# Optimization experiments

Hardware: AMD Instinct MI355X
Metric: run time of the kernel (lower is better)

Reference implementation:

```python
import jax, jax.numpy as jnp
import numpy as np

BATCH = 65536
SEQ_LEN = 32
EMB = 64
H = 128


def setup_inputs() -> dict:
    key = jax.random.key(0)
    ks = jax.random.split(key, 12)
    s = 0.05
    inp = {
        "last_pos": jax.random.normal(ks[0], (BATCH, 2), jnp.float32),
        "last_pos_rel": jax.random.normal(ks[1], (BATCH, 2), jnp.float32),
        "hh": jax.random.normal(ks[2], (1, BATCH, H), jnp.float32),
        "ch": jax.random.normal(ks[3], (1, BATCH, H), jnp.float32),
        "seq_start_end": jnp.sort(jax.random.randint(ks[4], (256, 2), 0, BATCH), axis=0),
        # LSTM(embedding_dim -> h_dim), PyTorch gate order [i, f, g, o]
        "w_ih": jax.random.normal(ks[5], (4 * H, EMB), jnp.float32) * s,
        "w_hh": jax.random.normal(ks[6], (4 * H, H), jnp.float32) * s,
        "b_ih": jax.random.normal(ks[7], (4 * H,), jnp.float32) * s,
        "b_hh": jax.random.normal(ks[8], (4 * H,), jnp.float32) * s,
        # spatial_embedding: Linear(2 -> EMB)
        "w_emb": jax.random.normal(ks[9], (EMB, 2), jnp.float32) * s,
        "b_emb": jax.random.normal(ks[10], (EMB,), jnp.float32) * s,
        # hidden2pos: Linear(H -> 2)
        "w_pos": jax.random.normal(ks[11], (2, H), jnp.float32) * s,
        "b_pos": jnp.zeros((2,), jnp.float32),
    }
    return inp


def _decode(last_pos, last_pos_rel, hh, ch, w_ih, w_hh, b_ih, b_hh,
            w_emb, b_emb, w_pos, b_pos):
    h0, c0 = hh[0], ch[0]                      # (B, H)
    x0 = last_pos_rel @ w_emb.T + b_emb        # (B, EMB)
    b = b_ih + b_hh

    def step(carry, _):
        h, c, lp, x = carry
        gates = x @ w_ih.T + h @ w_hh.T + b    # (B, 4H)
        i, f, g, o = jnp.split(gates, 4, axis=-1)
        c2 = jax.nn.sigmoid(f) * c + jax.nn.sigmoid(i) * jnp.tanh(g)
        h2 = jax.nn.sigmoid(o) * jnp.tanh(c2)
        rel = h2 @ w_pos.T + b_pos             # (B, 2)
        cur = rel + lp
        x2 = rel @ w_emb.T + b_emb             # next decoder input embedding
        return (h2, c2, cur, x2), rel

    (hN, cN, _, _), rels = jax.lax.scan(step, (h0, c0, last_pos, x0),
                                        None, length=SEQ_LEN)
    # rels: (SEQ_LEN, B, 2) == pred_traj_fake_rel; hN[None]: (1, B, H)
    return rels, hN[None]


def reference(last_pos, last_pos_rel, hh, ch, seq_start_end,
              w_ih, w_hh, b_ih, b_hh, w_emb, b_emb, w_pos, b_pos):
    # seq_start_end is unused when pool_every_timestep=False
    return _decode(last_pos, last_pos_rel, hh, ch,
                   w_ih, w_hh, b_ih, b_hh, w_emb, b_emb, w_pos, b_pos)
```

## Files before the change

### kernel.cpp

```cpp
#include <hip/hip_runtime.h>

#define B_TOT 65536
#define SEQ   32

typedef __bf16 bf16_8 __attribute__((ext_vector_type(8)));
typedef __bf16 bf16_4 __attribute__((ext_vector_type(4)));
typedef float  float4v __attribute__((ext_vector_type(4)));
typedef float  float2v __attribute__((ext_vector_type(2)));

#define SC1 (-1.4426950408889634f)
#define SC2 (-2.8853900817779268f)

__device__ inline unsigned short f2bf(float f){
    unsigned u = __builtin_bit_cast(unsigned, f);
    u += 0x7FFFu + ((u >> 16) & 1u);
    return (unsigned short)(u >> 16);
}

__device__ inline float2v v_exp2(float2v x){
    float2v r; r[0] = __builtin_amdgcn_exp2f(x[0]); r[1] = __builtin_amdgcn_exp2f(x[1]); return r;
}
__device__ inline float2v v_rcp(float2v x){
    float2v r; r[0] = __builtin_amdgcn_rcpf(x[0]); r[1] = __builtin_amdgcn_rcpf(x[1]); return r;
}
__device__ inline float2v v_fma(float2v a, float2v b, float2v c){
    float2v r; r[0] = __builtin_fmaf(a[0], b[0], c[0]); r[1] = __builtin_fmaf(a[1], b[1], c[1]); return r;
}

__global__ void prep_kernel(const float* __restrict__ w_ih,
                            const float* __restrict__ w_hh,
                            const float* __restrict__ b_ih,
                            const float* __restrict__ b_hh,
                            const float* __restrict__ w_emb,
                            const float* __restrict__ b_emb,
                            const float* __restrict__ w_pos,
                            const float* __restrict__ b_pos,
                            unsigned short* __restrict__ weff,
                            float* __restrict__ beff,
                            float* __restrict__ m2,
                            unsigned short* __restrict__ wposA)
{
    int n = threadIdx.x;
    float m20 = 0.f, m21 = 0.f, bi = 0.f;
    for (int e = 0; e < 64; ++e){
        float wv = w_ih[n*64 + e];
        m20 += w_emb[e*2 + 0] * wv;
        m21 += w_emb[e*2 + 1] * wv;
        bi  += b_emb[e] * wv;
    }
    float sc = ((n >> 7) == 2) ? SC2 : SC1;
    m2[n]       = m20 * sc;
    m2[512 + n] = m21 * sc;
    beff[n] = (b_ih[n] + b_hh[n] + bi + b_pos[0]*m20 + b_pos[1]*m21) * sc;
    for (int k = 0; k < 128; ++k){
        float wv = w_hh[n*128 + k] + w_pos[k]*m20 + w_pos[128 + k]*m21;
        weff[n*128 + k] = f2bf(wv * sc);
    }
    if (n < 256) wposA[n] = f2bf(w_pos[n]);
    for (int idx = n; idx < 14*128; idx += 512) wposA[256 + idx] = 0;
}

__global__ __launch_bounds__(256, 1) void dec_kernel(
    const float* __restrict__ lpr,
    const float* __restrict__ hh,
    const float* __restrict__ ch,
    const float* __restrict__ b_pos,
    const unsigned short* __restrict__ wposA,
    const unsigned short* __restrict__ weff,
    const float* __restrict__ beff,
    const float* __restrict__ m2,
    float* __restrict__ out)
{
    __shared__ __align__(16) unsigned short lhA[16][152];
    __shared__ __align__(16) unsigned short lhB[16][152];
    __shared__ float ubuf[32][2];
    __shared__ __align__(16) float hsh[32][132];

    const int tid  = threadIdx.x;
    const int w    = tid >> 6;
    const int lane = tid & 63;
    const int q    = lane >> 4;
    const int l    = lane & 15;
    const int row0 = blockIdx.x << 5;
    const int batchA = row0 + l;
    const int batchB = row0 + 16 + l;

    const float2v one2 = {1.f, 1.f};
    const float2v sc22 = {SC2, SC2};

    bf16_8 wA[8][4];
    float4v bias4[8];
#pragma unroll
    for (int t8 = 0; t8 < 8; ++t8){
        int nbase = ((t8 >> 1) << 7) + 32*w + ((t8 & 1) << 4);
        int gA = nbase + l;
#pragma unroll
        for (int kt = 0; kt < 4; ++kt)
            wA[t8][kt] = *(const bf16_8*)(weff + (gA << 7) + kt*32 + (q << 3));
        bias4[t8] = *(const float4v*)(beff + nbase + (q << 2));
    }

    bf16_8 wpA[4];
#pragma unroll
    for (int kt = 0; kt < 4; ++kt)
        wpA[kt] = *(const bf16_8*)(wposA + (l << 7) + kt*32 + (q << 3));
    const float bp0 = b_pos[0], bp1 = b_pos[1];

    float2v cstA[2][2], cstB[2][2];
#pragma unroll
    for (int X = 0; X < 2; ++X){
        float4v ca = *(const float4v*)(ch + (batchA << 7) + 32*w + 16*X + (q << 2));
        float4v cb = *(const float4v*)(ch + (batchB << 7) + 32*w + 16*X + (q << 2));
        float2v t;
        t[0]=ca[0]; t[1]=ca[1]; cstA[X][0]=t;
        t[0]=ca[2]; t[1]=ca[3]; cstA[X][1]=t;
        t[0]=cb[0]; t[1]=cb[1]; cstB[X][0]=t;
        t[0]=cb[2]; t[1]=cb[3]; cstB[X][1]=t;
    }

    bf16_8 bA[4], bB[4];
#pragma unroll
    for (int kt = 0; kt < 4; ++kt){
        const float* pa = hh + (batchA << 7) + kt*32 + (q << 3);
        const float* pb = hh + (batchB << 7) + kt*32 + (q << 3);
        float4v a0 = *(const float4v*)pa;      float4v a1 = *(const float4v*)(pa + 4);
        float4v c0 = *(const float4v*)pb;      float4v c1 = *(const float4v*)(pb + 4);
        bf16_8 ta, tb;
        ta[0]=(__bf16)a0[0]; ta[1]=(__bf16)a0[1]; ta[2]=(__bf16)a0[2]; ta[3]=(__bf16)a0[3];
        ta[4]=(__bf16)a1[0]; ta[5]=(__bf16)a1[1]; ta[6]=(__bf16)a1[2]; ta[7]=(__bf16)a1[3];
        tb[0]=(__bf16)c0[0]; tb[1]=(__bf16)c0[1]; tb[2]=(__bf16)c0[2]; tb[3]=(__bf16)c0[3];
        tb[4]=(__bf16)c1[0]; tb[5]=(__bf16)c1[1]; tb[6]=(__bf16)c1[2]; tb[7]=(__bf16)c1[3];
        bA[kt] = ta;
        bB[kt] = tb;
    }

    if (w == 0){
        float4v r = {0.f, 0.f, 0.f, 0.f};
#pragma unroll
        for (int kt = 0; kt < 4; ++kt)
            r = __builtin_amdgcn_mfma_f32_16x16x32_bf16(wpA[kt], bA[kt], r, 0, 0, 0);
        if (q == 0){
            float2v lp = *(const float2v*)(lpr + (batchA << 1));
            ubuf[l][0] = lp[0] - (r[0] + bp0);
            ubuf[l][1] = lp[1] - (r[1] + bp1);
        }
    }
    if (w == 1){
        float4v r = {0.f, 0.f, 0.f, 0.f};
#pragma unroll
        for (int kt = 0; kt < 4; ++kt)
            r = __builtin_amdgcn_mfma_f32_16x16x32_bf16(wpA[kt], bB[kt], r, 0, 0, 0);
        if (q == 0){
            float2v lp = *(const float2v*)(lpr + (batchB << 1));
            ubuf[16 + l][0] = lp[0] - (r[0] + bp0);
            ubuf[16 + l][1] = lp[1] - (r[1] + bp1);
        }
    }
    __syncthreads();

    float4v accA[8], accB[8];

    auto do_gates = [&](float4v (&acc)[8], bf16_8 (&b)[4]){
#pragma unroll
        for (int t8 = 0; t8 < 8; ++t8)
            acc[t8] = __builtin_amdgcn_mfma_f32_16x16x32_bf16(wA[t8][0], b[0], bias4[t8], 0, 0, 0);
#pragma unroll
        for (int kt = 1; kt < 4; ++kt)
#pragma unroll
            for (int t8 = 0; t8 < 8; ++t8)
                acc[t8] = __builtin_amdgcn_mfma_f32_16x16x32_bf16(wA[t8][kt], b[kt], acc[t8], 0, 0, 0);
    };

    auto u0fix = [&](float4v (&acc)[8], int ur){
        float u0 = ubuf[ur][0], u1 = ubuf[ur][1];
#pragma unroll
        for (int t8 = 0; t8 < 8; ++t8){
            int g0 = ((t8 >> 1) << 7) + 32*w + ((t8 & 1) << 4) + (q << 2);
            float4v ma = *(const float4v*)(m2 + g0);
            float4v mb = *(const float4v*)(m2 + 512 + g0);
#pragma unroll
            for (int r4 = 0; r4 < 4; ++r4)
                acc[t8][r4] += u0*ma[r4] + u1*mb[r4];
        }
    };

    auto elem_write = [&](float4v (&acc)[8], float2v (&cst)[2][2],
                          unsigned short (*lhp)[152], bool finalh, int hrow){
#pragma unroll
        for (int X = 0; X < 2; ++X){
            bf16_4 hv;
#pragma unroll
            for (int p = 0; p < 2; ++p){
                float2v iv = {acc[0 + X][2*p], acc[0 + X][2*p + 1]};
                float2v fv = {acc[2 + X][2*p], acc[2 + X][2*p + 1]};
                float2v gv = {acc[4 + X][2*p], acc[4 + X][2*p + 1]};
                float2v ov = {acc[6 + X][2*p], acc[6 + X][2*p + 1]};
                float2v ei = v_exp2(iv);
                float2v ef = v_exp2(fv);
                float2v eg = v_exp2(gv);
                float2v pi_ = ei + one2;
                float2v pf  = ef + one2;
                float2v pg  = eg + one2;
                float2v mg  = one2 - eg;
                float2v t2  = pi_ * pg;
                float2v den = pf * t2;
                float2v num = v_fma(cst[X][p], t2, pf * mg);
                float2v c2  = num * v_rcp(den);
                float2v eo  = v_exp2(ov);
                float2v ec  = v_exp2(c2 * sc22);
                float2v po  = eo + one2;
                float2v pc  = ec + one2;
                float2v mc  = one2 - ec;
                float2v h2  = mc * v_rcp(po * pc);
                cst[X][p] = c2;
                hv[2*p]     = (__bf16)h2[0];
                hv[2*p + 1] = (__bf16)h2[1];
                if (finalh){
                    int cb = 32*w + 16*X + (q << 2) + 2*p;
                    hsh[hrow][cb]     = h2[0];
                    hsh[hrow][cb + 1] = h2[1];
                }
            }
            *(bf16_4*)&lhp[l][32*w + 16*X + (q << 2)] = hv;
        }
    };

    auto reload = [&](bf16_8 (&b)[4], const unsigned short (*lhp)[152]){
#pragma unroll
        for (int kt = 0; kt < 4; ++kt)
            b[kt] = *(const bf16_8*)&lhp[l][kt*32 + (q << 3)];
    };

    auto relout = [&](bf16_8 (&b)[4], int t, int batch){
        float4v r = {0.f, 0.f, 0.f, 0.f};
#pragma unroll
        for (int kt = 0; kt < 4; ++kt)
            r = __builtin_amdgcn_mfma_f32_16x16x32_bf16(wpA[kt], b[kt], r, 0, 0, 0);
        if (q == 0){
            float2v rv;
            rv[0] = r[0] + bp0;
            rv[1] = r[1] + bp1;
            *(float2v*)(out + t*(B_TOT*2) + (batch << 1)) = rv;
        }
    };

    do_gates(accA, bA);
    u0fix(accA, l);

    for (int t = 0; t < SEQ; ++t){
        do_gates(accB, bB);
        if (t == 0) u0fix(accB, 16 + l);
        elem_write(accA, cstA, lhA, t == SEQ - 1, l);
        __syncthreads();
        reload(bA, lhA);
        if (w == (t & 3)) relout(bA, t, batchA);
        if (t < SEQ - 1) do_gates(accA, bA);
        elem_write(accB, cstB, lhB, t == SEQ - 1, 16 + l);
        __syncthreads();
        reload(bB, lhB);
        if (w == ((t + 2) & 3)) relout(bB, t, batchB);
    }

    __syncthreads();
    {
        int r = tid >> 3, c16 = (tid & 7) << 4;
        float4v v0 = *(const float4v*)&hsh[r][c16];
        float4v v1 = *(const float4v*)&hsh[r][c16 + 4];
        float4v v2 = *(const float4v*)&hsh[r][c16 + 8];
        float4v v3 = *(const float4v*)&hsh[r][c16 + 12];
        float* po = out + SEQ*B_TOT*2 + ((row0 + r) << 7) + c16;
        *(float4v*)po = v0;
        *(float4v*)(po + 4)  = v1;
        *(float4v*)(po + 8)  = v2;
        *(float4v*)(po + 12) = v3;
    }
}

extern "C" void kernel_launch(void* const* d_in, const int* in_sizes, int n_in,
                              void* d_out, int out_size, void* d_ws, size_t ws_size,
                              hipStream_t stream)
{
    (void)in_sizes; (void)n_in; (void)out_size; (void)ws_size;

    const float* lpr   = (const float*)d_in[1];
    const float* hh    = (const float*)d_in[2];
    const float* ch    = (const float*)d_in[3];
    const float* w_ih  = (const float*)d_in[5];
    const float* w_hh  = (const float*)d_in[6];
    const float* b_ih  = (const float*)d_in[7];
    const float* b_hh  = (const float*)d_in[8];
    const float* w_emb = (const float*)d_in[9];
    const float* b_emb = (const float*)d_in[10];
    const float* w_pos = (const float*)d_in[11];
    const float* b_pos = (const float*)d_in[12];

    unsigned short* weff  = (unsigned short*)d_ws;
    float* beff           = (float*)((char*)d_ws + 131072);
    float* m2             = (float*)((char*)d_ws + 131072 + 2048);
    unsigned short* wposA = (unsigned short*)((char*)d_ws + 131072 + 2048 + 4096);

    hipLaunchKernelGGL(prep_kernel, dim3(1), dim3(512), 0, stream,
                       w_ih, w_hh, b_ih, b_hh, w_emb, b_emb, w_pos, b_pos,
                       weff, beff, m2, wposA);
    hipLaunchKernelGGL(dec_kernel, dim3(B_TOT/32), dim3(256), 0, stream,
                       lpr, hh, ch, b_pos, wposA, weff, beff, m2,
                       (float*)d_out);
}
```

Measured before the change: 602.3 us.

## Split gate columns across eight waves per block instead of four

Each block now runs 512 threads (8 waves), and each wave owns 16 hidden columns per gate instead of 32. That halves per-thread weight registers, accumulators and cell state, and launch bounds now ask for two blocks per CU. The goal is more waves in flight, so MFMA and transcendental latency across the sequential timesteps can be hidden. In exchange, syncthreads barriers now span twice as many waves, and the per-block h reload from LDS is duplicated across more waves.

Measured after the change: 566.8 us. 1.06x faster.

```diff
diff --git a/kernel.cpp b/kernel.cpp
--- a/kernel.cpp
+++ b/kernel.cpp
@@ -60,7 +60,7 @@
     for (int idx = n; idx < 14*128; idx += 512) wposA[256 + idx] = 0;
 }
 
-__global__ __launch_bounds__(256, 1) void dec_kernel(
+__global__ __launch_bounds__(512, 2) void dec_kernel(
     const float* __restrict__ lpr,
     const float* __restrict__ hh,
     const float* __restrict__ ch,
@@ -88,16 +88,16 @@
     const float2v one2 = {1.f, 1.f};
     const float2v sc22 = {SC2, SC2};
 
-    bf16_8 wA[8][4];
-    float4v bias4[8];
-#pragma unroll
-    for (int t8 = 0; t8 < 8; ++t8){
-        int nbase = ((t8 >> 1) << 7) + 32*w + ((t8 & 1) << 4);
+    bf16_8 wA[4][4];
+    float4v bias4[4];
+#pragma unroll
+    for (int g = 0; g < 4; ++g){
+        int nbase = (g << 7) + (w << 4);
         int gA = nbase + l;
 #pragma unroll
         for (int kt = 0; kt < 4; ++kt)
-            wA[t8][kt] = *(const bf16_8*)(weff + (gA << 7) + kt*32 + (q << 3));
-        bias4[t8] = *(const float4v*)(beff + nbase + (q << 2));
+            wA[g][kt] = *(const bf16_8*)(weff + (gA << 7) + kt*32 + (q << 3));
+        bias4[g] = *(const float4v*)(beff + nbase + (q << 2));
     }
 
     bf16_8 wpA[4];
@@ -106,16 +106,15 @@
         wpA[kt] = *(const bf16_8*)(wposA + (l << 7) + kt*32 + (q << 3));
     const float bp0 = b_pos[0], bp1 = b_pos[1];
 
-    float2v cstA[2][2], cstB[2][2];
-#pragma unroll
-    for (int X = 0; X < 2; ++X){
-        float4v ca = *(const float4v*)(ch + (batchA << 7) + 32*w + 16*X + (q << 2));
-        float4v cb = *(const float4v*)(ch + (batchB << 7) + 32*w + 16*X + (q << 2));
+    float2v cstA[2], cstB[2];
+    {
+        float4v ca = *(const float4v*)(ch + (batchA << 7) + (w << 4) + (q << 2));
+        float4v cb = *(const float4v*)(ch + (batchB << 7) + (w << 4) + (q << 2));
         float2v t;
-        t[0]=ca[0]; t[1]=ca[1]; cstA[X][0]=t;
-        t[0]=ca[2]; t[1]=ca[3]; cstA[X][1]=t;
-        t[0]=cb[0]; t[1]=cb[1]; cstB[X][0]=t;
-        t[0]=cb[2]; t[1]=cb[3]; cstB[X][1]=t;
+        t[0]=ca[0]; t[1]=ca[1]; cstA[0]=t;
+        t[0]=ca[2]; t[1]=ca[3]; cstA[1]=t;
+        t[0]=cb[0]; t[1]=cb[1]; cstB[0]=t;
+        t[0]=cb[2]; t[1]=cb[3]; cstB[1]=t;
     }
 
     bf16_8 bA[4], bB[4];
@@ -158,71 +157,68 @@
     }
     __syncthreads();
 
-    float4v accA[8], accB[8];
-
-    auto do_gates = [&](float4v (&acc)[8], bf16_8 (&b)[4]){
-#pragma unroll
-        for (int t8 = 0; t8 < 8; ++t8)
-            acc[t8] = __builtin_amdgcn_mfma_f32_16x16x32_bf16(wA[t8][0], b[0], bias4[t8], 0, 0, 0);
+    float4v accA[4], accB[4];
+
+    auto do_gates = [&](float4v (&acc)[4], bf16_8 (&b)[4]){
+#pragma unroll
+        for (int g = 0; g < 4; ++g)
+            acc[g] = __builtin_amdgcn_mfma_f32_16x16x32_bf16(wA[g][0], b[0], bias4[g], 0, 0, 0);
 #pragma unroll
         for (int kt = 1; kt < 4; ++kt)
 #pragma unroll
-            for (int t8 = 0; t8 < 8; ++t8)
-                acc[t8] = __builtin_amdgcn_mfma_f32_16x16x32_bf16(wA[t8][kt], b[kt], acc[t8], 0, 0, 0);
-    };
-
-    auto u0fix = [&](float4v (&acc)[8], int ur){
+            for (int g = 0; g < 4; ++g)
+                acc[g] = __builtin_amdgcn_mfma_f32_16x16x32_bf16(wA[g][kt], b[kt], acc[g], 0, 0, 0);
+    };
+
+    auto u0fix = [&](float4v (&acc)[4], int ur){
         float u0 = ubuf[ur][0], u1 = ubuf[ur][1];
 #pragma unroll
-        for (int t8 = 0; t8 < 8; ++t8){
-            int g0 = ((t8 >> 1) << 7) + 32*w + ((t8 & 1) << 4) + (q << 2);
+        for (int g = 0; g < 4; ++g){
+            int g0 = (g << 7) + (w << 4) + (q << 2);
             float4v ma = *(const float4v*)(m2 + g0);
             float4v mb = *(const float4v*)(m2 + 512 + g0);
 #pragma unroll
             for (int r4 = 0; r4 < 4; ++r4)
-                acc[t8][r4] += u0*ma[r4] + u1*mb[r4];
-        }
-    };
-
-    auto elem_write = [&](float4v (&acc)[8], float2v (&cst)[2][2],
+                acc[g][r4] += u0*ma[r4] + u1*mb[r4];
+        }
+    };
+
+    auto elem_write = [&](float4v (&acc)[4], float2v (&cst)[2],
                           unsigned short (*lhp)[152], bool finalh, int hrow){
-#pragma unroll
-        for (int X = 0; X < 2; ++X){
-            bf16_4 hv;
-#pragma unroll
-            for (int p = 0; p < 2; ++p){
-                float2v iv = {acc[0 + X][2*p], acc[0 + X][2*p + 1]};
-                float2v fv = {acc[2 + X][2*p], acc[2 + X][2*p + 1]};
-                float2v gv = {acc[4 + X][2*p], acc[4 + X][2*p + 1]};
-                float2v ov = {acc[6 + X][2*p], acc[6 + X][2*p + 1]};
-                float2v ei = v_exp2(iv);
-                float2v ef = v_exp2(fv);
-                float2v eg = v_exp2(gv);
-                float2v pi_ = ei + one2;
-                float2v pf  = ef + one2;
-                float2v pg  = eg + one2;
-                float2v mg  = one2 - eg;
-                float2v t2  = pi_ * pg;
-                float2v den = pf * t2;
-                float2v num = v_fma(cst[X][p], t2, pf * mg);
-                float2v c2  = num * v_rcp(den);
-                float2v eo  = v_exp2(ov);
-                float2v ec  = v_exp2(c2 * sc22);
-                float2v po  = eo + one2;
-                float2v pc  = ec + one2;
-                float2v mc  = one2 - ec;
-                float2v h2  = mc * v_rcp(po * pc);
-                cst[X][p] = c2;
-                hv[2*p]     = (__bf16)h2[0];
-                hv[2*p + 1] = (__bf16)h2[1];
-                if (finalh){
-                    int cb = 32*w + 16*X + (q << 2) + 2*p;
-                    hsh[hrow][cb]     = h2[0];
-                    hsh[hrow][cb + 1] = h2[1];
-                }
+        bf16_4 hv;
+#pragma unroll
+        for (int p = 0; p < 2; ++p){
+            float2v iv = {acc[0][2*p], acc[0][2*p + 1]};
+            float2v fv = {acc[1][2*p], acc[1][2*p + 1]};
+            float2v gv = {acc[2][2*p], acc[2][2*p + 1]};
+            float2v ov = {acc[3][2*p], acc[3][2*p + 1]};
+            float2v ei = v_exp2(iv);
+            float2v ef = v_exp2(fv);
+            float2v eg = v_exp2(gv);
+            float2v pi_ = ei + one2;
+            float2v pf  = ef + one2;
+            float2v pg  = eg + one2;
+            float2v mg  = one2 - eg;
+            float2v t2  = pi_ * pg;
+            float2v den = pf * t2;
+            float2v num = v_fma(cst[p], t2, pf * mg);
+            float2v c2  = num * v_rcp(den);
+            float2v eo  = v_exp2(ov);
+            float2v ec  = v_exp2(c2 * sc22);
+            float2v po  = eo + one2;
+            float2v pc  = ec + one2;
+            float2v mc  = one2 - ec;
+            float2v h2  = mc * v_rcp(po * pc);
+            cst[p] = c2;
+            hv[2*p]     = (__bf16)h2[0];
+            hv[2*p + 1] = (__bf16)h2[1];
+            if (finalh){
+                int cb = (w << 4) + (q << 2) + 2*p;
+                hsh[hrow][cb]     = h2[0];
+                hsh[hrow][cb + 1] = h2[1];
             }
-            *(bf16_4*)&lhp[l][32*w + 16*X + (q << 2)] = hv;
-        }
+        }
+        *(bf16_4*)&lhp[l][(w << 4) + (q << 2)] = hv;
     };
 
     auto reload = [&](bf16_8 (&b)[4], const unsigned short (*lhp)[152]){
@@ -253,26 +249,22 @@
         elem_write(accA, cstA, lhA, t == SEQ - 1, l);
         __syncthreads();
         reload(bA, lhA);
-        if (w == (t & 3)) relout(bA, t, batchA);
+        if (w == (t & 7)) relout(bA, t, batchA);
         if (t < SEQ - 1) do_gates(accA, bA);
         elem_write(accB, cstB, lhB, t == SEQ - 1, 16 + l);
         __syncthreads();
         reload(bB, lhB);
-        if (w == ((t + 2) & 3)) relout(bB, t, batchB);
+        if (w == ((t + 4) & 7)) relout(bB, t, batchB);
     }
 
     __syncthreads();
     {
-        int r = tid >> 3, c16 = (tid & 7) << 4;
-        float4v v0 = *(const float4v*)&hsh[r][c16];
-        float4v v1 = *(const float4v*)&hsh[r][c16 + 4];
-        float4v v2 = *(const float4v*)&hsh[r][c16 + 8];
-        float4v v3 = *(const float4v*)&hsh[r][c16 + 12];
-        float* po = out + SEQ*B_TOT*2 + ((row0 + r) << 7) + c16;
+        int r = tid >> 4, c8 = (tid & 15) << 3;
+        float4v v0 = *(const float4v*)&hsh[r][c8];
+        float4v v1 = *(const float4v*)&hsh[r][c8 + 4];
+        float* po = out + SEQ*B_TOT*2 + ((row0 + r) << 7) + c8;
         *(float4v*)po = v0;
-        *(float4v*)(po + 4)  = v1;
-        *(float4v*)(po + 8)  = v2;
-        *(float4v*)(po + 12) = v3;
+        *(float4v*)(po + 4) = v1;
     }
 }
 
@@ -302,7 +294,7 @@
     hipLaunchKernelGGL(prep_kernel, dim3(1), dim3(512), 0, stream,
                        w_ih, w_hh, b_ih, b_hh, w_emb, b_emb, w_pos, b_pos,
                        weff, beff, m2, wposA);
-    hipLaunchKernelGGL(dec_kernel, dim3(B_TOT/32), dim3(256), 0, stream,
+    hipLaunchKernelGGL(dec_kernel, dim3(B_TOT/32), dim3(512), 0, stream,
                        lpr, hh, ch, b_pos, wposA, weff, beff, m2,
                        (float*)d_out);
 }
```
